# Kernel tuning notes

Hardware: AMD Instinct MI355X
Metric: run time of the kernel (lower is better)

The kernel has to match this reference:

```python
import jax, jax.numpy as jnp
import numpy as np

N_NODES = 20000
N_EDGES = 320000
N_GRAPHS = 256
D = 256
L = 4
EPS = 1e-5


def setup_inputs() -> dict:
    key = jax.random.key(0)
    ks = jax.random.split(key, 20)
    x = jax.random.normal(ks[0], (N_NODES, D), dtype=jnp.float32)
    edge_index = jax.random.randint(ks[1], (2, N_EDGES), 0, N_NODES, dtype=jnp.int64)
    batch = jnp.sort(jax.random.randint(ks[2], (N_NODES,), 0, N_GRAPHS, dtype=jnp.int64))
    s = 1.0 / np.sqrt(D)
    Wl = jax.random.uniform(ks[3], (L, D, D), jnp.float32, -s, s)
    bl = jax.random.uniform(ks[4], (L, D), jnp.float32, -s, s)
    Wr = jax.random.uniform(ks[5], (L, D, D), jnp.float32, -s, s)
    gamma = jnp.ones((L, D), jnp.float32)
    beta = jnp.zeros((L, D), jnp.float32)
    fc1_w = jax.random.uniform(ks[6], (D, 128), jnp.float32, -s, s)
    fc1_b = jax.random.uniform(ks[7], (128,), jnp.float32, -s, s)
    s2 = 1.0 / np.sqrt(128)
    fc2_w = jax.random.uniform(ks[8], (128, 64), jnp.float32, -s2, s2)
    fc2_b = jax.random.uniform(ks[9], (64,), jnp.float32, -s2, s2)
    s3 = 1.0 / np.sqrt(64)
    fc3_w = jax.random.uniform(ks[10], (64, 10), jnp.float32, -s3, s3)
    fc3_b = jax.random.uniform(ks[11], (10,), jnp.float32, -s3, s3)
    return dict(x=x, edge_index=edge_index, batch=batch, Wl=Wl, bl=bl, Wr=Wr,
                gamma=gamma, beta=beta, fc1_w=fc1_w, fc1_b=fc1_b,
                fc2_w=fc2_w, fc2_b=fc2_b, fc3_w=fc3_w, fc3_b=fc3_b)


def reference(x, edge_index, batch, Wl, bl, Wr, gamma, beta,
              fc1_w, fc1_b, fc2_w, fc2_b, fc3_w, fc3_b):
    src, dst = edge_index[0], edge_index[1]
    # in-degree for mean aggregation (zero-degree nodes -> 0 aggregate)
    deg = jax.ops.segment_sum(jnp.ones((src.shape[0],), x.dtype), dst, num_segments=N_NODES)
    inv_deg = jnp.where(deg > 0, 1.0 / jnp.maximum(deg, 1.0), 0.0)[:, None]
    for i in range(L):
        # SAGEConv: mean-aggregate neighbors, then lin_l(agg) + lin_r(x)
        agg = jax.ops.segment_sum(x[src], dst, num_segments=N_NODES) * inv_deg
        h = agg @ Wl[i] + bl[i] + x @ Wr[i]
        # BatchNorm (training mode: biased batch statistics over nodes)
        mu = jnp.mean(h, axis=0)
        var = jnp.mean(jnp.square(h - mu), axis=0)
        h = (h - mu) * jax.lax.rsqrt(var + EPS) * gamma[i] + beta[i]
        x = jax.nn.relu(h)
    # global_mean_pool over graphs
    cnt = jax.ops.segment_sum(jnp.ones((N_NODES,), x.dtype), batch, num_segments=N_GRAPHS)
    g = jax.ops.segment_sum(x, batch, num_segments=N_GRAPHS) / jnp.maximum(cnt, 1.0)[:, None]
    # MLP classifier: 256 -> 128 -> 64 -> 10
    g = jax.nn.relu(g @ fc1_w + fc1_b)
    g = jax.nn.relu(g @ fc2_w + fc2_b)
    return g @ fc3_w + fc3_b
```

## Files before the change

### kernel.cpp

```cpp
#include <hip/hip_runtime.h>
#include <hip/hip_bf16.h>

#define NN 20000
#define NE 320000
#define NG 256
#define DD 256
#define NL 4
#define NBKT 79
#define BM 80
#define NBLK 250

typedef __attribute__((ext_vector_type(8))) short short8;
typedef __attribute__((ext_vector_type(4))) float float4_t;

__device__ __forceinline__ int ld_idx(const int* __restrict__ p, int i, int f64) {
    return f64 ? p[2 * i] : p[i];
}

__device__ __forceinline__ float bf2f(ushort u) {
    return __uint_as_float(((unsigned)u) << 16);
}

__device__ __forceinline__ ushort f2bf(float f) {
    __hip_bfloat16 b = __float2bfloat16(f);
    return *(ushort*)&b;
}


__global__ void k_init(const int* __restrict__ ei, const int* __restrict__ batch,
                       const ushort* __restrict__ x, int* __restrict__ flags,
                       int* __restrict__ deg) {
    int gid = blockIdx.x * 256 + threadIdx.x;
    for (int i = gid; i < NN; i += gridDim.x * 256) deg[i] = 0;
    if (blockIdx.x == 0) {
        __shared__ int cnt0, cnt1, weird;
        int t = threadIdx.x;
        if (t == 0) { cnt0 = 0; cnt1 = 0; weird = 0; }
        __syncthreads();
        for (int tt = t; tt < 512; tt += 256) {
            if (ei[2 * tt + 1] != 0) atomicAdd(&cnt0, 1);
            int i = tt * 9;
            if (batch[2 * i + 1] != 0) atomicAdd(&cnt1, 1);
#pragma unroll
            for (int j = 0; j < 16; j++) {
                ushort v = x[tt * 16 + j];
                if (((v >> 7) & 0xFF) >= 0xC0) atomicAdd(&weird, 1);
            }
        }
        __syncthreads();
        if (t == 0) {
            flags[0] = (cnt0 == 0) ? 1 : 0;
            flags[1] = (cnt1 == 0) ? 1 : 0;
            flags[2] = (weird == 0) ? 1 : 0;
        }
    }
}


#define POFF_BL   0
#define POFF_GA   1024
#define POFF_BE   2048
#define POFF_F1W  3072
#define POFF_F1B  35840
#define POFF_F2W  35968
#define POFF_F2B  44160
#define POFF_F3W  44224
#define POFF_F3B  44864
#define PTOT      44874

#define NB_CVT8   2500
#define NB_FRAG   128
#define NB_CVTP   176
#define NB_DEG    1250
#define NB_GST    79
#define B_FRAG    (NB_CVT8)
#define B_CVTP    (B_FRAG + NB_FRAG)
#define B_DEG     (B_CVTP + NB_CVTP)
#define B_GST     (B_DEG + NB_DEG)
#define NB_PREP   (B_GST + NB_GST)


__global__ __launch_bounds__(256) void k_prep(
    const void* __restrict__ x_in, const void* __restrict__ WL,
    const void* __restrict__ WR, const int* __restrict__ ei,
    const int* __restrict__ batch,
    const void* s0, const void* s1, const void* s2, const void* s3,
    const void* s4, const void* s5, const void* s6, const void* s7, const void* s8,
    ushort* __restrict__ xcan, ushort* __restrict__ wtL, ushort* __restrict__ wtR,
    ushort* __restrict__ pcan, int* __restrict__ deg, int* __restrict__ gstart,
    const int* __restrict__ fl) {
    int blk = blockIdx.x;
    int t = threadIdx.x;
    if (blk < B_FRAG) {
        int i = blk * 256 + t;
        if (fl[2]) {
            *(int4*)(xcan + (size_t)i * 8) = ((const int4*)x_in)[i];
        } else {
            const float* f = (const float*)x_in + (size_t)i * 8;
            ushort ov[8];
#pragma unroll
            for (int d = 0; d < 8; d++) ov[d] = f2bf(f[d]);
            *(int4*)(xcan + (size_t)i * 8) = *(int4*)ov;
        }
    } else if (blk < B_CVTP) {
        __shared__ ushort T[64][65];
        int bid = blk - B_FRAG;
        int lm = bid >> 4;
        int tile = bid & 15;
        int tk = (tile >> 2) * 64, tn = (tile & 3) * 64;
        const void* W = (lm >= 4) ? WR : WL;
        ushort* Wt = (lm >= 4) ? wtR : wtL;
        size_t base = (size_t)(lm & 3) << 16;
        int f32 = !fl[2];
#pragma unroll
        for (int i = 0; i < 16; i++) {
            int flat = t + i * 256;
            int r = flat >> 6, c = flat & 63;
            size_t src = base + (size_t)(tk + r) * 256 + tn + c;
            ushort v = f32 ? f2bf(((const float*)W)[src]) : ((const ushort*)W)[src];
            T[c][r] = v;
        }
        __syncthreads();
#pragma unroll
        for (int i = 0; i < 2; i++) {
            int slot = t + i * 256;
            int f = slot >> 6;
            int lane = slot & 63;
            int ln = (f >> 1) * 16 + (lane & 15);
            int lk = (f & 1) * 32 + ((lane >> 4) << 3);
            int gfblk = ((tn + ln) >> 4) * 8 + ((tk + lk) >> 5);
            ushort tmp[8];
#pragma unroll
            for (int j = 0; j < 8; j++) tmp[j] = T[ln][lk + j];
            *(int4*)(Wt + base + (size_t)gfblk * 512 + lane * 8) = *(int4*)tmp;
        }
    } else if (blk < B_DEG) {
        int i = (blk - B_CVTP) * 256 + t;
        if (i >= PTOT) return;
        const int offs[10] = {POFF_BL, POFF_GA, POFF_BE, POFF_F1W, POFF_F1B,
                              POFF_F2W, POFF_F2B, POFF_F3W, POFF_F3B, PTOT};
        const void* srcs[9] = {s0, s1, s2, s3, s4, s5, s6, s7, s8};
        int seg = 0;
#pragma unroll
        for (int k = 1; k < 9; k++) if (i >= offs[k]) seg = k;
        int local = i - offs[seg];
        if (fl[2]) pcan[i] = ((const ushort*)srcs[seg])[local];
        else       pcan[i] = f2bf(((const float*)srcs[seg])[local]);
    } else if (blk < B_GST) {
        int e = (blk - B_CVTP - NB_CVTP) * 256 + t;
        e = (blk - B_DEG) * 256 + t;
        if (e < NE) {
            int src = ld_idx(ei, e, fl[0]);
            int dst = ld_idx(ei, NE + e, fl[0]);
            if ((unsigned)dst < NN && (unsigned)src < NN) atomicAdd(&deg[dst], 1);
        }
    } else {
        int i = (blk - B_GST) * 256 + t;
        if (i >= NN) return;
        int b = ld_idx(batch, i, fl[1]);
        int bp = (i == 0) ? -1 : ld_idx(batch, i - 1, fl[1]);
        for (int g = bp + 1; g <= b; g++)
            if ((unsigned)g <= NG) gstart[g] = i;
        if (i == NN - 1)
            for (int g = b + 1; g <= NG; g++) gstart[g] = NN;
    }
}


__global__ __launch_bounds__(256) void k_scan(
    const int* __restrict__ deg, int* __restrict__ rowst,
    int* __restrict__ cursor, float* __restrict__ invdeg) {
    __shared__ int red[256];
    __shared__ int part[256];
    int b = blockIdx.x, t = threadIdx.x;
    int s = 0;
    for (int i = t; i < b * 256; i += 256) s += deg[i];
    red[t] = s;
    __syncthreads();
    for (int off = 128; off; off >>= 1) {
        if (t < off) red[t] += red[t + off];
        __syncthreads();
    }
    int bpref = red[0];
    int node = b * 256 + t;
    int d = (node < NN) ? deg[node] : 0;
    part[t] = d;
    __syncthreads();
    for (int off = 1; off < 256; off <<= 1) {
        int v = (t >= off) ? part[t - off] : 0;
        __syncthreads();
        part[t] += v;
        __syncthreads();
    }
    if (node < NN) {
        int o = bpref + part[t] - d;
        rowst[node] = o;
        cursor[node] = o;
        invdeg[node] = d > 0 ? 1.0f / (float)d : 0.0f;
    }
    if (b == NBKT - 1 && t == 255) rowst[NN] = bpref + part[255];
}

__global__ void k_fill(const int* __restrict__ ei, int* __restrict__ cursor,
                       int* __restrict__ csr, const int* __restrict__ fl) {
    int e = blockIdx.x * 256 + threadIdx.x;
    if (e < NE) {
        int src = ld_idx(ei, e, fl[0]);
        int dst = ld_idx(ei, NE + e, fl[0]);
        if ((unsigned)dst < NN && (unsigned)src < NN) {
            int p = atomicAdd(&cursor[dst], 1);
            if ((unsigned)p < NE) csr[p] = src;
        }
    }
}


template <int BNF>
__global__ __launch_bounds__(256) void k_agg4(
    const ushort* __restrict__ X, const int* __restrict__ rs,
    const int* __restrict__ csr, const float* __restrict__ invdeg,
    const float* __restrict__ bnsc, const float* __restrict__ bnsh,
    ushort* __restrict__ AGG) {
    int node = blockIdx.x * 4 + (threadIdx.x >> 6);
    if (node >= NN) return;
    int h = (threadIdx.x >> 5) & 1;
    int j = threadIdx.x & 31;
    float sc[8], sh[8];
    if (BNF) {
        float4 a0 = *(const float4*)(bnsc + j * 8);
        float4 a1 = *(const float4*)(bnsc + j * 8 + 4);
        float4 b0 = *(const float4*)(bnsh + j * 8);
        float4 b1 = *(const float4*)(bnsh + j * 8 + 4);
        sc[0] = a0.x; sc[1] = a0.y; sc[2] = a0.z; sc[3] = a0.w;
        sc[4] = a1.x; sc[5] = a1.y; sc[6] = a1.z; sc[7] = a1.w;
        sh[0] = b0.x; sh[1] = b0.y; sh[2] = b0.z; sh[3] = b0.w;
        sh[4] = b1.x; sh[5] = b1.y; sh[6] = b1.z; sh[7] = b1.w;
    }
    int e0 = rs[node], e1 = rs[node + 1];
    float acc[8] = {};
    int e = e0 + h;
    for (; e + 14 < e1; e += 16) {
        int4 v[8];
#pragma unroll
        for (int r = 0; r < 8; r++) {
            int s = csr[e + 2 * r];
            v[r] = *(const int4*)(X + (size_t)s * DD + j * 8);
        }
#pragma unroll
        for (int r = 0; r < 8; r++) {
            const ushort* u = (const ushort*)&v[r];
#pragma unroll
            for (int d = 0; d < 8; d++) {
                float x = bf2f(u[d]);
                if (BNF) x = fmaxf(x * sc[d] + sh[d], 0.0f);
                acc[d] += x;
            }
        }
    }
    for (; e + 2 < e1; e += 4) {
        int sA = csr[e], sB = csr[e + 2];
        int4 vA = *(const int4*)(X + (size_t)sA * DD + j * 8);
        int4 vB = *(const int4*)(X + (size_t)sB * DD + j * 8);
        const ushort* uA = (const ushort*)&vA;
        const ushort* uB = (const ushort*)&vB;
#pragma unroll
        for (int d = 0; d < 8; d++) {
            float xA = bf2f(uA[d]), xB = bf2f(uB[d]);
            if (BNF) {
                xA = fmaxf(xA * sc[d] + sh[d], 0.0f);
                xB = fmaxf(xB * sc[d] + sh[d], 0.0f);
            }
            acc[d] += xA + xB;
        }
    }
    for (; e < e1; e += 2) {
        int s = csr[e];
        int4 v = *(const int4*)(X + (size_t)s * DD + j * 8);
        const ushort* u = (const ushort*)&v;
#pragma unroll
        for (int d = 0; d < 8; d++) {
            float x = bf2f(u[d]);
            if (BNF) x = fmaxf(x * sc[d] + sh[d], 0.0f);
            acc[d] += x;
        }
    }
#pragma unroll
    for (int d = 0; d < 8; d++)
        acc[d] += __shfl_down(acc[d], 32);
    if (h == 0) {
        float inv = invdeg[node];
        ushort ov[8];
#pragma unroll
        for (int d = 0; d < 8; d++) ov[d] = f2bf(acc[d] * inv);
        *(int4*)(AGG + (size_t)node * DD + j * 8) = *(int4*)ov;
    }
}


template <int BNF>
__global__ __launch_bounds__(256) void k_gemm6(
    const ushort* __restrict__ A1, const ushort* __restrict__ A2,
    const ushort* __restrict__ WtF1, const ushort* __restrict__ WtF2,
    const ushort* __restrict__ bias,
    const float* __restrict__ bnsc, const float* __restrict__ bnsh,
    ushort* __restrict__ H, float* __restrict__ psum, float* __restrict__ psq) {
    __shared__ ushort Als[BM][264];
    __shared__ float colsum[128];
    __shared__ float colsq[128];
    const int m0 = blockIdx.x * BM;
    const int n0 = blockIdx.y * 128;
    const int tid = threadIdx.x;
    const int w = tid >> 6, lane = tid & 63;
    const int lr = lane & 15, q = lane >> 4;
    float4_t acc[5][2] = {};

    if (tid < 128) { colsum[tid] = 0.0f; colsq[tid] = 0.0f; }

    for (int mat = 0; mat < 2; ++mat) {
        const ushort* A = mat ? A2 : A1;
        const ushort* Wf = mat ? WtF2 : WtF1;
        __syncthreads();
#pragma unroll
        for (int i = 0; i < 10; i++) {
            int flat = tid + i * 256;
            int r = flat >> 5;
            int c = (flat & 31) * 8;
            int4 av = *(const int4*)(A + (size_t)(m0 + r) * DD + c);
            if (BNF && mat == 1) {
                ushort* u = (ushort*)&av;
#pragma unroll
                for (int d = 0; d < 8; d++)
                    u[d] = f2bf(fmaxf(bf2f(u[d]) * bnsc[c + d] + bnsh[c + d], 0.0f));
            }
            *(int4*)&Als[r][c] = av;
        }
        __syncthreads();
#pragma unroll
        for (int k0 = 0; k0 < 256; k0 += 32) {
            short8 af[5];
#pragma unroll
            for (int im = 0; im < 5; im++)
                af[im] = *(const short8*)&Als[im * 16 + lr][k0 + q * 8];
            const ushort* bbase =
                Wf + (((size_t)(((n0 + w * 32) >> 4) * 8 + (k0 >> 5))) << 9) + lane * 8;
#pragma unroll
            for (int in = 0; in < 2; in++) {
                short8 bf = *(const short8*)(bbase + in * 4096);
#pragma unroll
                for (int im = 0; im < 5; im++)
                    acc[im][in] = __builtin_amdgcn_mfma_f32_16x16x32_bf16(
                        af[im], bf, acc[im][in], 0, 0, 0);
            }
        }
    }

    const int mbase = m0 + q * 4;
#pragma unroll
    for (int in = 0; in < 2; ++in) {
        const int nl = w * 32 + in * 16 + lr;
        const int n = n0 + nl;
        float b = bf2f(bias[n]);
        float s = 0.0f, s2 = 0.0f;
#pragma unroll
        for (int im = 0; im < 5; ++im) {
#pragma unroll
            for (int i = 0; i < 4; ++i) {
                int m = mbase + im * 16 + i;
                float hv = acc[im][in][i] + b;
                ushort hb = f2bf(hv);
                H[(size_t)m * DD + n] = hb;
                float hq = bf2f(hb);
                s += hq;
                s2 += hq * hq;
            }
        }
        s += __shfl_xor(s, 16);  s += __shfl_xor(s, 32);
        s2 += __shfl_xor(s2, 16); s2 += __shfl_xor(s2, 32);
        if (q == 0) {
            atomicAdd(&colsum[nl], s);
            atomicAdd(&colsq[nl], s2);
        }
    }
    __syncthreads();
    if (tid < 128) {
        psum[(size_t)blockIdx.x * DD + n0 + tid] = colsum[tid];
        psq[(size_t)blockIdx.x * DD + n0 + tid] = colsq[tid];
    }
}


__global__ __launch_bounds__(64) void k_bnfinal3(
    const float* __restrict__ psum, const float* __restrict__ psq,
    const ushort* __restrict__ gamma, const ushort* __restrict__ beta,
    float* __restrict__ scale, float* __restrict__ shift) {
    int c = blockIdx.x;
    int t = threadIdx.x;
    float s = 0.0f, s2 = 0.0f;
    for (int b = t; b < NBLK; b += 64) {
        s += psum[(size_t)b * DD + c];
        s2 += psq[(size_t)b * DD + c];
    }
#pragma unroll
    for (int o = 32; o; o >>= 1) {
        s += __shfl_down(s, o);
        s2 += __shfl_down(s2, o);
    }
    if (t == 0) {
        float mu = s * (1.0f / NN);
        float var = s2 * (1.0f / NN) - mu * mu;
        if (var < 0.0f) var = 0.0f;
        float rstd = rsqrtf(var + 1e-5f);
        float g = bf2f(gamma[c]);
        float b2 = bf2f(beta[c]);
        scale[c] = g * rstd;
        shift[c] = b2 - mu * g * rstd;
    }
}


__global__ __launch_bounds__(256) void k_head(
    const ushort* __restrict__ Hb, const float* __restrict__ scale,
    const float* __restrict__ shift, const int* __restrict__ gstart,
    const ushort* __restrict__ fc1w, const ushort* __restrict__ fc1b,
    const ushort* __restrict__ fc2w, const ushort* __restrict__ fc2b,
    const ushort* __restrict__ fc3w, const ushort* __restrict__ fc3b,
    void* __restrict__ out, const int* __restrict__ fl) {
    __shared__ float g[256];
    __shared__ float h1[128];
    __shared__ float h2[64];
    int gid = blockIdx.x;
    int t = threadIdx.x;
    int s0 = gstart[gid], e = gstart[gid + 1];
    float sc = scale[t], sh = shift[t];
    float acc = 0.0f;
    for (int i = s0; i < e; i++)
        acc += fmaxf(bf2f(Hb[(size_t)i * DD + t]) * sc + sh, 0.0f);
    g[t] = acc / fmaxf((float)(e - s0), 1.0f);
    __syncthreads();
    if (t < 128) {
        float a = bf2f(fc1b[t]);
        for (int k = 0; k < 256; k++)
            a += g[k] * bf2f(fc1w[k * 128 + t]);
        h1[t] = fmaxf(a, 0.0f);
    }
    __syncthreads();
    if (t < 64) {
        float a2 = bf2f(fc2b[t]);
        for (int k = 0; k < 128; k++)
            a2 += h1[k] * bf2f(fc2w[k * 64 + t]);
        h2[t] = fmaxf(a2, 0.0f);
    }
    __syncthreads();
    if (t < 10) {
        float a3 = bf2f(fc3b[t]);
        for (int k = 0; k < 64; k++)
            a3 += h2[k] * bf2f(fc3w[k * 10 + t]);
        if (fl[2]) ((__hip_bfloat16*)out)[gid * 10 + t] = __float2bfloat16(a3);
        else       ((float*)out)[gid * 10 + t] = a3;
    }
}


static inline char* bump(char*& p, size_t n) {
    char* r = p;
    p += (n + 255) & ~(size_t)255;
    return r;
}

extern "C" void kernel_launch(void* const* d_in, const int* in_sizes, int n_in,
                              void* d_out, int out_size, void* d_ws, size_t ws_size,
                              hipStream_t stream) {
    const void* x_in  = d_in[0];
    const int*  ei    = (const int*)d_in[1];
    const int*  batch = (const int*)d_in[2];
    const void* Wl    = d_in[3];
    const void* bl    = d_in[4];
    const void* Wr    = d_in[5];
    const void* gamma = d_in[6];
    const void* beta  = d_in[7];

    char* p = (char*)d_ws;
    int*    flags    = (int*)bump(p, 256);
    ushort* wtL      = (ushort*)bump(p, (size_t)NL * 65536 * 2);
    ushort* wtR      = (ushort*)bump(p, (size_t)NL * 65536 * 2);
    ushort* xcan     = (ushort*)bump(p, (size_t)NN * DD * 2);
    ushort* pcan     = (ushort*)bump(p, (size_t)PTOT * 2);
    int*    deg      = (int*)bump(p, NN * 4);
    int*    rowst    = (int*)bump(p, (NN + 1) * 4);
    int*    cursor   = (int*)bump(p, NN * 4);
    float*  invdeg   = (float*)bump(p, NN * 4);
    int*    csr      = (int*)bump(p, NE * 4);
    int*    gstart   = (int*)bump(p, (NG + 1) * 4);
    ushort* agg      = (ushort*)bump(p, (size_t)NN * DD * 2);
    ushort* hb0      = (ushort*)bump(p, (size_t)NN * DD * 2);
    ushort* hb1      = (ushort*)bump(p, (size_t)NN * DD * 2);
    float*  psum     = (float*)bump(p, (size_t)NBLK * DD * 4);
    float*  psq      = (float*)bump(p, (size_t)NBLK * DD * 4);
    float*  scale    = (float*)bump(p, DD * 4);
    float*  shift    = (float*)bump(p, DD * 4);

    if ((size_t)(p - (char*)d_ws) > ws_size) return;

    ushort* blc = pcan + POFF_BL;
    ushort* gac = pcan + POFF_GA;
    ushort* bec = pcan + POFF_BE;
    ushort* f1w = pcan + POFF_F1W;
    ushort* f1b = pcan + POFF_F1B;
    ushort* f2w = pcan + POFF_F2W;
    ushort* f2b = pcan + POFF_F2B;
    ushort* f3w = pcan + POFF_F3W;
    ushort* f3b = pcan + POFF_F3B;

    k_init<<<80, 256, 0, stream>>>(ei, batch, (const ushort*)x_in, flags, deg);
    k_prep<<<NB_PREP, 256, 0, stream>>>(
        x_in, Wl, Wr, ei, batch,
        bl, gamma, beta, d_in[8], d_in[9], d_in[10], d_in[11], d_in[12], d_in[13],
        xcan, wtL, wtR, pcan, deg, gstart, flags);
    k_scan<<<NBKT, 256, 0, stream>>>(deg, rowst, cursor, invdeg);
    k_fill<<<(NE + 255) / 256, 256, 0, stream>>>(ei, cursor, csr, flags);

    ushort* hbuf[2] = {hb0, hb1};
    const ushort* xsrc = xcan;
    for (int l = 0; l < NL; l++) {
        ushort* hdst = hbuf[l & 1];
        const ushort* wl = wtL + (size_t)l * 65536;
        const ushort* wr = wtR + (size_t)l * 65536;
        if (l == 0) {
            k_agg4<0><<<(NN + 3) / 4, 256, 0, stream>>>(xsrc, rowst, csr, invdeg,
                                                        scale, shift, agg);
            k_gemm6<0><<<dim3(NBLK, 2), 256, 0, stream>>>(
                agg, xsrc, wl, wr, blc, scale, shift, hdst, psum, psq);
        } else {
            k_agg4<1><<<(NN + 3) / 4, 256, 0, stream>>>(xsrc, rowst, csr, invdeg,
                                                        scale, shift, agg);
            k_gemm6<1><<<dim3(NBLK, 2), 256, 0, stream>>>(
                agg, xsrc, wl, wr, blc + l * DD, scale, shift, hdst, psum, psq);
        }
        k_bnfinal3<<<DD, 64, 0, stream>>>(psum, psq, gac + l * DD, bec + l * DD,
                                          scale, shift);
        xsrc = hdst;
    }

    k_head<<<NG, 256, 0, stream>>>(xsrc, scale, shift, gstart,
                                   f1w, f1b, f2w, f2b, f3w, f3b, d_out, flags);
}
```

Baseline: 366.6 us.

## Fuse BatchNorm finalize into GEMM via last-block reduction and cache head weights in LDS

Removes the separate per-layer BN-finalize kernel. Each GEMM block writes its column partial sums in a transposed layout and bumps a global atomic counter. The last block to finish reduces all partials, writes the scale/shift buffers and resets the counter, which saves one launch per layer but puts a serial reduction on the tail of each GEMM. The head kernel now copies the three MLP weight matrices into shared memory, unrolls the pooling loop by 8 and unrolls the dot products, at the cost of each block loading about 80KB into LDS.

```diff
diff --git a/kernel.cpp b/kernel.cpp
--- a/kernel.cpp
+++ b/kernel.cpp
@@ -9,6 +9,7 @@
 #define NBKT 79
 #define BM 80
 #define NBLK 250
+#define NGB 500
 
 typedef __attribute__((ext_vector_type(8))) short short8;
 typedef __attribute__((ext_vector_type(4))) float float4_t;
@@ -29,9 +30,10 @@
 
 __global__ void k_init(const int* __restrict__ ei, const int* __restrict__ batch,
                        const ushort* __restrict__ x, int* __restrict__ flags,
-                       int* __restrict__ deg) {
+                       int* __restrict__ deg, int* __restrict__ gctr) {
     int gid = blockIdx.x * 256 + threadIdx.x;
     for (int i = gid; i < NN; i += gridDim.x * 256) deg[i] = 0;
+    if (gid == 0) *gctr = 0;
     if (blockIdx.x == 0) {
         __shared__ int cnt0, cnt1, weird;
         int t = threadIdx.x;
@@ -147,8 +149,7 @@
         if (fl[2]) pcan[i] = ((const ushort*)srcs[seg])[local];
         else       pcan[i] = f2bf(((const float*)srcs[seg])[local]);
     } else if (blk < B_GST) {
-        int e = (blk - B_CVTP - NB_CVTP) * 256 + t;
-        e = (blk - B_DEG) * 256 + t;
+        int e = (blk - B_DEG) * 256 + t;
         if (e < NE) {
             int src = ld_idx(ei, e, fl[0]);
             int dst = ld_idx(ei, NE + e, fl[0]);
@@ -298,15 +299,18 @@
 
 
 template <int BNF>
-__global__ __launch_bounds__(256) void k_gemm6(
+__global__ __launch_bounds__(256) void k_gemm7(
     const ushort* __restrict__ A1, const ushort* __restrict__ A2,
     const ushort* __restrict__ WtF1, const ushort* __restrict__ WtF2,
     const ushort* __restrict__ bias,
     const float* __restrict__ bnsc, const float* __restrict__ bnsh,
-    ushort* __restrict__ H, float* __restrict__ psum, float* __restrict__ psq) {
+    ushort* __restrict__ H, float* __restrict__ psumT, float* __restrict__ psqT,
+    const ushort* __restrict__ gamma, const ushort* __restrict__ beta,
+    float* __restrict__ scale, float* __restrict__ shift, int* __restrict__ ctr) {
     __shared__ ushort Als[BM][264];
     __shared__ float colsum[128];
     __shared__ float colsq[128];
+    __shared__ int isLast;
     const int m0 = blockIdx.x * BM;
     const int n0 = blockIdx.y * 128;
     const int tid = threadIdx.x;
@@ -383,38 +387,45 @@
     }
     __syncthreads();
     if (tid < 128) {
-        psum[(size_t)blockIdx.x * DD + n0 + tid] = colsum[tid];
-        psq[(size_t)blockIdx.x * DD + n0 + tid] = colsq[tid];
-    }
-}
-
-
-__global__ __launch_bounds__(64) void k_bnfinal3(
-    const float* __restrict__ psum, const float* __restrict__ psq,
-    const ushort* __restrict__ gamma, const ushort* __restrict__ beta,
-    float* __restrict__ scale, float* __restrict__ shift) {
-    int c = blockIdx.x;
-    int t = threadIdx.x;
-    float s = 0.0f, s2 = 0.0f;
-    for (int b = t; b < NBLK; b += 64) {
-        s += psum[(size_t)b * DD + c];
-        s2 += psq[(size_t)b * DD + c];
-    }
-#pragma unroll
-    for (int o = 32; o; o >>= 1) {
-        s += __shfl_down(s, o);
-        s2 += __shfl_down(s2, o);
-    }
-    if (t == 0) {
-        float mu = s * (1.0f / NN);
-        float var = s2 * (1.0f / NN) - mu * mu;
-        if (var < 0.0f) var = 0.0f;
-        float rstd = rsqrtf(var + 1e-5f);
-        float g = bf2f(gamma[c]);
-        float b2 = bf2f(beta[c]);
-        scale[c] = g * rstd;
-        shift[c] = b2 - mu * g * rstd;
-    }
+        psumT[(size_t)(n0 + tid) * 256 + blockIdx.x] = colsum[tid];
+        psqT[(size_t)(n0 + tid) * 256 + blockIdx.x] = colsq[tid];
+    }
+
+    __threadfence();
+    if (tid == 0) isLast = (atomicAdd(ctr, 1) == NGB - 1);
+    __syncthreads();
+    if (!isLast) return;
+    __threadfence();
+    const int u = lane;
+#pragma unroll 4
+    for (int pass = 0; pass < 64; ++pass) {
+        int c = pass * 4 + w;
+        float s = 0.0f, s2 = 0.0f;
+#pragma unroll
+        for (int k = 0; k < 4; ++k) {
+            int b = u + 64 * k;
+            if (b < NBLK) {
+                s += psumT[(size_t)c * 256 + b];
+                s2 += psqT[(size_t)c * 256 + b];
+            }
+        }
+#pragma unroll
+        for (int o = 32; o; o >>= 1) {
+            s += __shfl_down(s, o);
+            s2 += __shfl_down(s2, o);
+        }
+        if (u == 0) {
+            float mu = s * (1.0f / NN);
+            float var = s2 * (1.0f / NN) - mu * mu;
+            if (var < 0.0f) var = 0.0f;
+            float rstd = rsqrtf(var + 1e-5f);
+            float g = bf2f(gamma[c]);
+            float b2 = bf2f(beta[c]);
+            scale[c] = g * rstd;
+            shift[c] = b2 - mu * g * rstd;
+        }
+    }
+    if (tid == 0) *ctr = 0;
 }
 
 
@@ -428,33 +439,51 @@
     __shared__ float g[256];
     __shared__ float h1[128];
     __shared__ float h2[64];
+    __shared__ ushort w1[256 * 128];
+    __shared__ ushort w2[128 * 64];
+    __shared__ ushort w3[64 * 10];
     int gid = blockIdx.x;
     int t = threadIdx.x;
+    for (int i = t; i < 256 * 128 / 8; i += 256) ((int4*)w1)[i] = ((const int4*)fc1w)[i];
+    for (int i = t; i < 128 * 64 / 8; i += 256) ((int4*)w2)[i] = ((const int4*)fc2w)[i];
+    if (t < 80) ((int4*)w3)[t] = ((const int4*)fc3w)[t];
+
     int s0 = gstart[gid], e = gstart[gid + 1];
     float sc = scale[t], sh = shift[t];
     float acc = 0.0f;
-    for (int i = s0; i < e; i++)
+    int i = s0;
+    for (; i + 7 < e; i += 8) {
+        float v[8];
+#pragma unroll
+        for (int r = 0; r < 8; r++) v[r] = bf2f(Hb[(size_t)(i + r) * DD + t]);
+#pragma unroll
+        for (int r = 0; r < 8; r++) acc += fmaxf(v[r] * sc + sh, 0.0f);
+    }
+    for (; i < e; i++)
         acc += fmaxf(bf2f(Hb[(size_t)i * DD + t]) * sc + sh, 0.0f);
     g[t] = acc / fmaxf((float)(e - s0), 1.0f);
     __syncthreads();
     if (t < 128) {
         float a = bf2f(fc1b[t]);
+#pragma unroll 8
         for (int k = 0; k < 256; k++)
-            a += g[k] * bf2f(fc1w[k * 128 + t]);
+            a += g[k] * bf2f(w1[k * 128 + t]);
         h1[t] = fmaxf(a, 0.0f);
     }
     __syncthreads();
     if (t < 64) {
         float a2 = bf2f(fc2b[t]);
+#pragma unroll 8
         for (int k = 0; k < 128; k++)
-            a2 += h1[k] * bf2f(fc2w[k * 64 + t]);
+            a2 += h1[k] * bf2f(w2[k * 64 + t]);
         h2[t] = fmaxf(a2, 0.0f);
     }
     __syncthreads();
     if (t < 10) {
         float a3 = bf2f(fc3b[t]);
+#pragma unroll 8
         for (int k = 0; k < 64; k++)
-            a3 += h2[k] * bf2f(fc3w[k * 10 + t]);
+            a3 += h2[k] * bf2f(w3[k * 10 + t]);
         if (fl[2]) ((__hip_bfloat16*)out)[gid * 10 + t] = __float2bfloat16(a3);
         else       ((float*)out)[gid * 10 + t] = a3;
     }
@@ -481,6 +510,7 @@
 
     char* p = (char*)d_ws;
     int*    flags    = (int*)bump(p, 256);
+    int*    gctr     = (int*)bump(p, 256);
     ushort* wtL      = (ushort*)bump(p, (size_t)NL * 65536 * 2);
     ushort* wtR      = (ushort*)bump(p, (size_t)NL * 65536 * 2);
     ushort* xcan     = (ushort*)bump(p, (size_t)NN * DD * 2);
@@ -494,8 +524,8 @@
     ushort* agg      = (ushort*)bump(p, (size_t)NN * DD * 2);
     ushort* hb0      = (ushort*)bump(p, (size_t)NN * DD * 2);
     ushort* hb1      = (ushort*)bump(p, (size_t)NN * DD * 2);
-    float*  psum     = (float*)bump(p, (size_t)NBLK * DD * 4);
-    float*  psq      = (float*)bump(p, (size_t)NBLK * DD * 4);
+    float*  psumT    = (float*)bump(p, (size_t)DD * 256 * 4);
+    float*  psqT     = (float*)bump(p, (size_t)DD * 256 * 4);
     float*  scale    = (float*)bump(p, DD * 4);
     float*  shift    = (float*)bump(p, DD * 4);
 
@@ -511,7 +541,7 @@
     ushort* f3w = pcan + POFF_F3W;
     ushort* f3b = pcan + POFF_F3B;
 
-    k_init<<<80, 256, 0, stream>>>(ei, batch, (const ushort*)x_in, flags, deg);
+    k_init<<<80, 256, 0, stream>>>(ei, batch, (const ushort*)x_in, flags, deg, gctr);
     k_prep<<<NB_PREP, 256, 0, stream>>>(
         x_in, Wl, Wr, ei, batch,
         bl, gamma, beta, d_in[8], d_in[9], d_in[10], d_in[11], d_in[12], d_in[13],
@@ -528,16 +558,16 @@
         if (l == 0) {
             k_agg4<0><<<(NN + 3) / 4, 256, 0, stream>>>(xsrc, rowst, csr, invdeg,
                                                         scale, shift, agg);
-            k_gemm6<0><<<dim3(NBLK, 2), 256, 0, stream>>>(
-                agg, xsrc, wl, wr, blc, scale, shift, hdst, psum, psq);
+            k_gemm7<0><<<dim3(NBLK, 2), 256, 0, stream>>>(
+                agg, xsrc, wl, wr, blc, scale, shift, hdst, psumT, psqT,
+                gac, bec, scale, shift, gctr);
         } else {
             k_agg4<1><<<(NN + 3) / 4, 256, 0, stream>>>(xsrc, rowst, csr, invdeg,
                                                         scale, shift, agg);
-            k_gemm6<1><<<dim3(NBLK, 2), 256, 0, stream>>>(
-                agg, xsrc, wl, wr, blc + l * DD, scale, shift, hdst, psum, psq);
-        }
-        k_bnfinal3<<<DD, 64, 0, stream>>>(psum, psq, gac + l * DD, bec + l * DD,
-                                          scale, shift);
+            k_gemm7<1><<<dim3(NBLK, 2), 256, 0, stream>>>(
+                agg, xsrc, wl, wr, blc + l * DD, scale, shift, hdst, psumT, psqT,
+                gac + l * DD, bec + l * DD, scale, shift, gctr);
+        }
         xsrc = hdst;
     }
 
```

After: 866.1 us. 2.36x slower.
